# Kernel optimization log

Hardware: AMD Instinct MI355X
Metric: run time of the kernel (lower is better)

The kernel has to match this reference:

```python
import jax, jax.numpy as jnp
import numpy as np

B, S, H, L = 64, 512, 768, 9


def setup_inputs() -> dict:
    key = jax.random.key(0)
    ks = jax.random.split(key, 8)
    hidden = jax.random.normal(ks[0], (B, S, H), jnp.float32)
    lengths = jax.random.randint(ks[1], (B,), S // 2, S + 1)
    attention_mask = (jnp.arange(S)[None, :] < lengths[:, None]).astype(jnp.int32)
    labels = jax.random.randint(ks[2], (B, S), 0, L)
    # sprinkle some -100 ignore labels like HF datasets do
    ignore = jax.random.uniform(ks[3], (B, S)) < 0.05
    labels = jnp.where(ignore, -100, labels)
    W = jax.random.normal(ks[4], (H, L), jnp.float32) * 0.02
    b = jnp.zeros((L,), jnp.float32)
    start_transitions = jax.random.uniform(ks[5], (L,), jnp.float32, -0.1, 0.1)
    end_transitions = jax.random.uniform(ks[6], (L,), jnp.float32, -0.1, 0.1)
    transitions = jax.random.uniform(ks[7], (L, L), jnp.float32, -0.1, 0.1)
    return dict(hidden=hidden, attention_mask=attention_mask, labels=labels, W=W, b=b,
                start_transitions=start_transitions, end_transitions=end_transitions,
                transitions=transitions)


def _crf_numerator(emissions, tags, maskf, start_t, end_t, trans):
    # score of the gold tag sequence (torchcrf _compute_score)
    first = start_t[tags[:, 0]] + jnp.take_along_axis(emissions[:, 0], tags[:, 0:1], axis=1)[:, 0]
    em = jnp.take_along_axis(emissions, tags[..., None], axis=2)[..., 0]      # [B,S]
    tr = trans[tags[:, :-1], tags[:, 1:]]                                     # [B,S-1]
    score = first + jnp.sum((em[:, 1:] + tr) * maskf[:, 1:], axis=1)
    last_idx = (jnp.sum(maskf, axis=1).astype(jnp.int32) - 1)
    last_tags = jnp.take_along_axis(tags, last_idx[:, None], axis=1)[:, 0]
    return score + end_t[last_tags]


def _crf_lognorm(emissions, maskf, start_t, end_t, trans):
    # forward algorithm (torchcrf _compute_normalizer) as a lax.scan
    score0 = start_t[None, :] + emissions[:, 0]                               # [B,L]
    em_seq = jnp.transpose(emissions[:, 1:], (1, 0, 2))                       # [S-1,B,L]
    m_seq = maskf[:, 1:].T                                                    # [S-1,B]

    def step(score, xs):
        em_t, m_t = xs
        nxt = jax.nn.logsumexp(score[:, :, None] + trans[None] + em_t[:, None, :], axis=1)
        return jnp.where(m_t[:, None] > 0, nxt, score), None

    score, _ = jax.lax.scan(step, score0, (em_seq, m_seq))
    return jax.nn.logsumexp(score + end_t[None, :], axis=1)


def _viterbi(emissions, maskf, start_t, end_t, trans):
    score0 = start_t[None, :] + emissions[:, 0]                               # [B,L]
    em_seq = jnp.transpose(emissions[:, 1:], (1, 0, 2))
    m_seq = maskf[:, 1:].T

    def step(score, xs):
        em_t, m_t = xs
        cand = score[:, :, None] + trans[None]                                # [B,L,L]
        bp = jnp.argmax(cand, axis=1)                                         # [B,L]
        nxt = jnp.max(cand, axis=1) + em_t
        return jnp.where(m_t[:, None] > 0, nxt, score), bp

    score, history = jax.lax.scan(step, score0, (em_seq, m_seq))              # history [S-1,B,L]
    best_last = jnp.argmax(score + end_t[None, :], axis=1)                    # [B]

    def back(cur, xs):
        bp_t, m_t = xs
        prev = jnp.where(m_t > 0, jnp.take_along_axis(bp_t, cur[:, None], axis=1)[:, 0], cur)
        return prev, prev

    _, tags_rev = jax.lax.scan(back, best_last, (history[::-1], m_seq[::-1]))
    tags = jnp.concatenate([tags_rev[::-1].T, best_last[:, None]], axis=1)    # [B,S]
    return tags


def reference(hidden, attention_mask, labels, W, b, start_transitions, end_transitions, transitions):
    maskf = attention_mask.astype(hidden.dtype)                               # [B,S]
    logits = jnp.einsum('bsh,hl->bsl', hidden, W) + b                         # [B,S,L]
    safe_labels = jnp.where(labels == -100, 0, labels)
    num = _crf_numerator(logits, safe_labels, maskf, start_transitions, end_transitions, transitions)
    den = _crf_lognorm(logits, maskf, start_transitions, end_transitions, transitions)
    loss = -jnp.mean(num - den)                                               # -crf(..., reduction='mean')
    tags = _viterbi(logits, maskf, start_transitions, end_transitions, transitions)
    fake_logits = jax.nn.one_hot(tags, L, dtype=logits.dtype) * maskf[..., None]
    return loss, fake_logits
```

## Files before the change

### kernel.cpp

```cpp
#include <hip/hip_runtime.h>
#include <hip/hip_bf16.h>
#include <stdint.h>

constexpr int BB  = 64;
constexpr int SS  = 512;
constexpr int HH  = 768;
constexpr int NL  = 9;
constexpr int NROWS = BB * SS;
constexpr int EMN   = SS * NL;
constexpr float L2E = 1.4426950408889634f;
constexpr float LN2 = 0.6931471805599453f;

__device__ __forceinline__ float readlane_f(float v, int lane) {
  union { float f; int i; } u;
  u.f = v;
  u.i = __builtin_amdgcn_readlane(u.i, lane);
  return u.f;
}

__global__ __launch_bounds__(256, 2) void logits_kernel(
    const float* __restrict__ hidden, const float* __restrict__ W,
    const float* __restrict__ bias, float* __restrict__ logits) {
  const int lane = threadIdx.x & 63;
  const int wid  = blockIdx.x * 4 + (threadIdx.x >> 6);

  float w[3][4][NL];
#pragma unroll
  for (int j = 0; j < 3; ++j)
#pragma unroll
    for (int k = 0; k < 4; ++k) {
      const int r = lane * 4 + j * 256 + k;
#pragma unroll
      for (int l = 0; l < NL; ++l) w[j][k][l] = W[r * NL + l];
    }
  const float my_bias = (lane < NL) ? bias[lane] : 0.0f;

#pragma unroll
  for (int rep = 0; rep < 2; ++rep) {
    const int rA = wid + rep * 16384;
    const int rB = rA + 8192;
    const float4* hA = (const float4*)(hidden + (size_t)rA * HH);
    const float4* hB = (const float4*)(hidden + (size_t)rB * HH);
    float accA[NL], accB[NL];
#pragma unroll
    for (int l = 0; l < NL; ++l) { accA[l] = 0.0f; accB[l] = 0.0f; }
#pragma unroll
    for (int j = 0; j < 3; ++j) {
      const float4 a = hA[lane + j * 64];
      const float4 b = hB[lane + j * 64];
#pragma unroll
      for (int l = 0; l < NL; ++l) {
        accA[l] += a.x * w[j][0][l] + a.y * w[j][1][l] +
                   a.z * w[j][2][l] + a.w * w[j][3][l];
        accB[l] += b.x * w[j][0][l] + b.y * w[j][1][l] +
                   b.z * w[j][2][l] + b.w * w[j][3][l];
      }
    }
#pragma unroll
    for (int off = 32; off >= 1; off >>= 1)
#pragma unroll
      for (int l = 0; l < NL; ++l) {
        accA[l] += __shfl_xor(accA[l], off, 64);
        accB[l] += __shfl_xor(accB[l], off, 64);
      }
    if (lane < NL) {
      float vA = accA[0], vB = accB[0];
#pragma unroll
      for (int l = 1; l < NL; ++l)
        if (lane == l) { vA = accA[l]; vB = accB[l]; }
      logits[(size_t)rA * NL + lane] = vA + my_bias;
      logits[(size_t)rB * NL + lane] = vB + my_bias;
    }
  }
}

__global__ __launch_bounds__(64) void crf_kernel(
    const float* __restrict__ logits, const int* __restrict__ mask,
    const int* __restrict__ labels, const float* __restrict__ start_t,
    const float* __restrict__ end_t, const float* __restrict__ trans,
    float* __restrict__ out, float* __restrict__ num_den) {
  __shared__ __align__(16) float em_s[EMN + 16];
  __shared__ float tr_s[NL * NL];
  __shared__ int   lab[SS];
  __shared__ unsigned char bp_s[EMN + 80];
  __shared__ unsigned char tags_s[SS];
  __shared__ int   len_s;

  const int role = blockIdx.x >> 6;
  const int b    = blockIdx.x & 63;
  const int tid  = threadIdx.x;
  const float esc = (role == 0) ? L2E : 1.0f;

  {
    const float4* src = (const float4*)(logits + (size_t)b * EMN);
    float4* dst = (float4*)em_s;
    for (int i = tid; i < EMN / 4; i += 64) {
      float4 v = src[i];
      v.x *= esc; v.y *= esc; v.z *= esc; v.w *= esc;
      dst[i] = v;
    }
  }
  for (int i = tid; i < NL * NL; i += 64) tr_s[i] = trans[i] * esc;
  int lsum = 0;
  for (int t = tid; t < SS; t += 64) lsum += mask[b * SS + t];
#pragma unroll
  for (int off = 32; off >= 1; off >>= 1) lsum += __shfl_xor(lsum, off, 64);
  if (tid == 0) len_s = lsum;
  if (role == 2) {
    for (int t = tid; t < SS; t += 64) {
      const int v = labels[b * SS + t];
      lab[t] = (v == -100) ? 0 : v;
    }
  }
  __syncthreads();
  const int len = len_s;

  if (role == 0) {
    const int j = (tid < NL) ? tid : 0;
    float tcol[NL];
#pragma unroll
    for (int i = 0; i < NL; ++i) tcol[i] = tr_s[i * NL + j];
    float s[NL];
#pragma unroll
    for (int i = 0; i < NL; ++i) s[i] = start_t[i] * L2E + em_s[i];
    float emj = em_s[NL + j];
    for (int t = 1; t < len; ++t) {
      const float emj_n = em_s[(t + 1) * NL + j];
      float c[NL];
#pragma unroll
      for (int i = 0; i < NL; ++i) c[i] = s[i] + tcol[i];
      const float m01 = fmaxf(c[0], c[1]), m23 = fmaxf(c[2], c[3]);
      const float m45 = fmaxf(c[4], c[5]), m67 = fmaxf(c[6], c[7]);
      const float m = fmaxf(fmaxf(fmaxf(m01, m23), fmaxf(m45, m67)), c[8]);
      float p[NL];
#pragma unroll
      for (int i = 0; i < NL; ++i) p[i] = exp2f(c[i] - m);
      const float s01 = p[0] + p[1], s23 = p[2] + p[3];
      const float s45 = p[4] + p[5], s67 = p[6] + p[7];
      const float sum = ((s01 + s23) + (s45 + s67)) + p[8];
      const float nxt = m + __log2f(sum) + emj;
#pragma unroll
      for (int i = 0; i < NL; ++i) s[i] = readlane_f(nxt, i);
      emj = emj_n;
    }
    float c[NL];
#pragma unroll
    for (int i = 0; i < NL; ++i) c[i] = s[i] + end_t[i] * L2E;
    const float m01 = fmaxf(c[0], c[1]), m23 = fmaxf(c[2], c[3]);
    const float m45 = fmaxf(c[4], c[5]), m67 = fmaxf(c[6], c[7]);
    const float m = fmaxf(fmaxf(fmaxf(m01, m23), fmaxf(m45, m67)), c[8]);
    float sum = 0.0f;
#pragma unroll
    for (int i = 0; i < NL; ++i) sum += exp2f(c[i] - m);
    if (tid == 0) num_den[64 + b] = (m + __log2f(sum)) * LN2;

  } else if (role == 1) {
    const int j = (tid < NL) ? tid : 0;
    float tcol[NL];
#pragma unroll
    for (int i = 0; i < NL; ++i) tcol[i] = tr_s[i * NL + j];
    float s[NL];
#pragma unroll
    for (int i = 0; i < NL; ++i) s[i] = start_t[i] + em_s[i];
    float emj = em_s[NL + j];
    for (int t = 1; t < len; ++t) {
      const float emj_n = em_s[(t + 1) * NL + j];
      float c[NL];
#pragma unroll
      for (int i = 0; i < NL; ++i) c[i] = s[i] + tcol[i];
      const bool b01 = c[0] >= c[1], b23 = c[2] >= c[3];
      const bool b45 = c[4] >= c[5], b67 = c[6] >= c[7];
      const float v01 = b01 ? c[0] : c[1]; const int i01 = b01 ? 0 : 1;
      const float v23 = b23 ? c[2] : c[3]; const int i23 = b23 ? 2 : 3;
      const float v45 = b45 ? c[4] : c[5]; const int i45 = b45 ? 4 : 5;
      const float v67 = b67 ? c[6] : c[7]; const int i67 = b67 ? 6 : 7;
      const bool bA = v01 >= v23, bB = v45 >= v67;
      const float vA = bA ? v01 : v23; const int iA = bA ? i01 : i23;
      const float vB = bB ? v45 : v67; const int iB = bB ? i45 : i67;
      const bool bC = vA >= vB;
      const float vC = bC ? vA : vB; const int iC = bC ? iA : iB;
      const bool bD = vC >= c[8];
      const float best = bD ? vC : c[8];
      const int   arg  = bD ? iC : 8;
      bp_s[t * NL + tid] = (unsigned char)arg;
      const float nxt = best + emj;
#pragma unroll
      for (int i = 0; i < NL; ++i) s[i] = readlane_f(nxt, i);
      emj = emj_n;
    }
    float bv = s[0] + end_t[0];
    int   bl = 0;
#pragma unroll
    for (int i = 1; i < NL; ++i) {
      const float cc = s[i] + end_t[i];
      if (cc > bv) { bv = cc; bl = i; }
    }
    __syncthreads();

    uint64_t C = 0x876543210ULL;
#pragma unroll
    for (int k = 1; k <= 8; ++k) {
      const int t = 8 * tid + k;
      uint64_t nc = 0;
#pragma unroll
      for (int x = 0; x < 9; ++x) {
        const int g = bp_s[t * NL + x] & 15;
        nc |= ((C >> (4 * g)) & 15ULL) << (4 * x);
      }
      C = (t < len) ? nc : C;
    }
    const uint32_t Clo = (uint32_t)C, Chi = (uint32_t)(C >> 32);
    uint32_t cur = (uint32_t)bl;
    int bnd = 0;
#pragma unroll
    for (int c = 63; c >= 0; --c) {
      bnd = (tid == c) ? (int)cur : bnd;
      const uint32_t lo = (uint32_t)__builtin_amdgcn_readlane((int)Clo, c);
      const uint32_t hi = (uint32_t)__builtin_amdgcn_readlane((int)Chi, c);
      const uint64_t cc = ((uint64_t)hi << 32) | lo;
      cur = (uint32_t)((cc >> (4 * cur)) & 15u);
    }
    int tag = bnd;
#pragma unroll
    for (int k = 8; k >= 1; --k) {
      const int t = 8 * tid + k;
      const int tt = (t < 512) ? t : 511;
      const int nt = bp_s[tt * NL + tag];
      tag = (t < len) ? nt : tag;
      tags_s[t - 1] = (unsigned char)tag;
    }
    __syncthreads();
    for (int i = tid; i < EMN; i += 64) {
      const int t = i / NL;
      const int l = i - t * NL;
      out[1 + (size_t)b * EMN + i] =
          (t < len && l == (int)tags_s[t]) ? 1.0f : 0.0f;
    }

  } else {
    float contrib = 0.0f;
    for (int t = tid; t < SS; t += 64) {
      if (t >= 1 && t < len)
        contrib += em_s[t * NL + lab[t]] + tr_s[lab[t - 1] * NL + lab[t]];
    }
#pragma unroll
    for (int off = 32; off >= 1; off >>= 1)
      contrib += __shfl_xor(contrib, off, 64);
    if (tid == 0) {
      const int l0 = lab[0];
      num_den[b] = start_t[l0] + em_s[l0] + contrib + end_t[lab[len - 1]];
    }
  }
}

__global__ __launch_bounds__(64) void loss_kernel(
    const float* __restrict__ num_den, float* __restrict__ out) {
  const int tid = threadIdx.x;
  float v = num_den[64 + tid] - num_den[tid];
#pragma unroll
  for (int off = 32; off >= 1; off >>= 1) v += __shfl_xor(v, off, 64);
  if (tid == 0) out[0] = v * (1.0f / 64.0f);
}

extern "C" void kernel_launch(void* const* d_in, const int* in_sizes, int n_in,
                              void* d_out, int out_size, void* d_ws, size_t ws_size,
                              hipStream_t stream) {
  const float* hidden  = (const float*)d_in[0];
  const int*   mask    = (const int*)d_in[1];
  const int*   labels  = (const int*)d_in[2];
  const float* W       = (const float*)d_in[3];
  const float* bias    = (const float*)d_in[4];
  const float* start_t = (const float*)d_in[5];
  const float* end_t   = (const float*)d_in[6];
  const float* trans   = (const float*)d_in[7];
  float* out = (float*)d_out;

  float* logits  = (float*)d_ws;
  float* num_den = logits + (size_t)NROWS * NL;

  logits_kernel<<<2048, 256, 0, stream>>>(hidden, W, bias, logits);
  crf_kernel<<<192, 64, 0, stream>>>(logits, mask, labels, start_t, end_t,
                                     trans, out, num_den);
  loss_kernel<<<1, 64, 0, stream>>>(num_den, out);
}
```

Measured before the change: 292.0 us.

## Parallelize CRF forward algorithm via segmented log-semiring transfer matrices

The sequential forward (log-normalizer) scan is split into 8 segments per batch, each computed from 9 one-hot starting states in separate blocks. A new combine kernel chains the resulting 9x9 log-space transfer matrices, so the serial recurrence depth drops from about 512 steps to about 64. Sequence lengths are now computed inside the logits kernel. Emissions are read directly from global memory with a 4-deep register prefetch instead of being staged in LDS. The change adds roughly 4.6k extra blocks of redundant work and another kernel launch, and uses fast __expf/__logf instead of the exp2/log2 scaling.

```diff
diff --git a/kernel.cpp b/kernel.cpp
--- a/kernel.cpp
+++ b/kernel.cpp
@@ -8,8 +8,8 @@
 constexpr int NL  = 9;
 constexpr int NROWS = BB * SS;
 constexpr int EMN   = SS * NL;
-constexpr float L2E = 1.4426950408889634f;
-constexpr float LN2 = 0.6931471805599453f;
+constexpr int NSEG  = 8;
+constexpr float NEG  = -1e30f;
 
 __device__ __forceinline__ float readlane_f(float v, int lane) {
   union { float f; int i; } u;
@@ -20,9 +20,20 @@
 
 __global__ __launch_bounds__(256, 2) void logits_kernel(
     const float* __restrict__ hidden, const float* __restrict__ W,
-    const float* __restrict__ bias, float* __restrict__ logits) {
+    const float* __restrict__ bias, const int* __restrict__ mask,
+    float* __restrict__ logits, int* __restrict__ lens) {
   const int lane = threadIdx.x & 63;
   const int wid  = blockIdx.x * 4 + (threadIdx.x >> 6);
+
+  if (blockIdx.x < 64 && threadIdx.x < 64) {
+    const int4* mp = (const int4*)(mask + blockIdx.x * SS);
+    const int4 a = mp[threadIdx.x];
+    const int4 c = mp[threadIdx.x + 64];
+    int lsum = a.x + a.y + a.z + a.w + c.x + c.y + c.z + c.w;
+#pragma unroll
+    for (int off = 32; off >= 1; off >>= 1) lsum += __shfl_xor(lsum, off, 64);
+    if (threadIdx.x == 0) lens[blockIdx.x] = lsum;
+  }
 
   float w[3][4][NL];
 #pragma unroll
@@ -74,119 +85,60 @@
   }
 }
 
-__global__ __launch_bounds__(64) void crf_kernel(
-    const float* __restrict__ logits, const int* __restrict__ mask,
-    const int* __restrict__ labels, const float* __restrict__ start_t,
-    const float* __restrict__ end_t, const float* __restrict__ trans,
-    float* __restrict__ out, float* __restrict__ num_den) {
-  __shared__ __align__(16) float em_s[EMN + 16];
-  __shared__ float tr_s[NL * NL];
-  __shared__ int   lab[SS];
+__global__ __launch_bounds__(64) void scan_kernel(
+    const float* __restrict__ logits, const int* __restrict__ labels,
+    const float* __restrict__ start_t, const float* __restrict__ end_t,
+    const float* __restrict__ trans, float* __restrict__ out,
+    float* __restrict__ num_den, const int* __restrict__ lens,
+    float* __restrict__ segmat) {
   __shared__ unsigned char bp_s[EMN + 80];
   __shared__ unsigned char tags_s[SS];
-  __shared__ int   len_s;
-
-  const int role = blockIdx.x >> 6;
-  const int b    = blockIdx.x & 63;
-  const int tid  = threadIdx.x;
-  const float esc = (role == 0) ? L2E : 1.0f;
-
-  {
-    const float4* src = (const float4*)(logits + (size_t)b * EMN);
-    float4* dst = (float4*)em_s;
-    for (int i = tid; i < EMN / 4; i += 64) {
-      float4 v = src[i];
-      v.x *= esc; v.y *= esc; v.z *= esc; v.w *= esc;
-      dst[i] = v;
-    }
-  }
-  for (int i = tid; i < NL * NL; i += 64) tr_s[i] = trans[i] * esc;
-  int lsum = 0;
-  for (int t = tid; t < SS; t += 64) lsum += mask[b * SS + t];
-#pragma unroll
-  for (int off = 32; off >= 1; off >>= 1) lsum += __shfl_xor(lsum, off, 64);
-  if (tid == 0) len_s = lsum;
-  if (role == 2) {
-    for (int t = tid; t < SS; t += 64) {
-      const int v = labels[b * SS + t];
-      lab[t] = (v == -100) ? 0 : v;
-    }
-  }
-  __syncthreads();
-  const int len = len_s;
-
-  if (role == 0) {
-    const int j = (tid < NL) ? tid : 0;
-    float tcol[NL];
-#pragma unroll
-    for (int i = 0; i < NL; ++i) tcol[i] = tr_s[i * NL + j];
+  __shared__ int lab[SS];
+
+  const int blk = blockIdx.x;
+  const int tid = threadIdx.x;
+  const int j   = (tid < NL) ? tid : NL - 1;
+
+  if (blk < 64) {
+    const int b   = blk;
+    const int len = lens[b];
+    const float* emb = logits + (size_t)b * EMN;
+    float tc[NL];
+#pragma unroll
+    for (int i = 0; i < NL; ++i) tc[i] = trans[i * NL + j];
     float s[NL];
 #pragma unroll
-    for (int i = 0; i < NL; ++i) s[i] = start_t[i] * L2E + em_s[i];
-    float emj = em_s[NL + j];
+    for (int i = 0; i < NL; ++i) s[i] = start_t[i] + emb[i];
+    float eA = emb[1 * NL + j], eB = emb[2 * NL + j];
+    float eC = emb[3 * NL + j], eD = emb[4 * NL + j];
     for (int t = 1; t < len; ++t) {
-      const float emj_n = em_s[(t + 1) * NL + j];
       float c[NL];
 #pragma unroll
-      for (int i = 0; i < NL; ++i) c[i] = s[i] + tcol[i];
-      const float m01 = fmaxf(c[0], c[1]), m23 = fmaxf(c[2], c[3]);
-      const float m45 = fmaxf(c[4], c[5]), m67 = fmaxf(c[6], c[7]);
-      const float m = fmaxf(fmaxf(fmaxf(m01, m23), fmaxf(m45, m67)), c[8]);
-      float p[NL];
-#pragma unroll
-      for (int i = 0; i < NL; ++i) p[i] = exp2f(c[i] - m);
-      const float s01 = p[0] + p[1], s23 = p[2] + p[3];
-      const float s45 = p[4] + p[5], s67 = p[6] + p[7];
-      const float sum = ((s01 + s23) + (s45 + s67)) + p[8];
-      const float nxt = m + __log2f(sum) + emj;
+      for (int i = 0; i < NL; ++i) c[i] = s[i] + tc[i];
+      const float x01 = fmaxf(c[0], c[1]), x23 = fmaxf(c[2], c[3]);
+      const float x45 = fmaxf(c[4], c[5]), x67 = fmaxf(c[6], c[7]);
+      const float best = fmaxf(fmaxf(fmaxf(x01, x23), fmaxf(x45, x67)), c[8]);
+      const float nxt = best + eA;
+      {
+        const bool b01 = c[0] >= c[1], b23 = c[2] >= c[3];
+        const bool b45 = c[4] >= c[5], b67 = c[6] >= c[7];
+        const float v01 = b01 ? c[0] : c[1]; const int i01 = b01 ? 0 : 1;
+        const float v23 = b23 ? c[2] : c[3]; const int i23 = b23 ? 2 : 3;
+        const float v45 = b45 ? c[4] : c[5]; const int i45 = b45 ? 4 : 5;
+        const float v67 = b67 ? c[6] : c[7]; const int i67 = b67 ? 6 : 7;
+        const bool bA = v01 >= v23, bB = v45 >= v67;
+        const float vA = bA ? v01 : v23; const int iA = bA ? i01 : i23;
+        const float vB = bB ? v45 : v67; const int iB = bB ? i45 : i67;
+        const bool bC = vA >= vB;
+        const float vC = bC ? vA : vB; const int iC = bC ? iA : iB;
+        const bool bD = vC >= c[8];
+        const int arg = bD ? iC : 8;
+        bp_s[t * NL + tid] = (unsigned char)arg;
+      }
 #pragma unroll
       for (int i = 0; i < NL; ++i) s[i] = readlane_f(nxt, i);
-      emj = emj_n;
-    }
-    float c[NL];
-#pragma unroll
-    for (int i = 0; i < NL; ++i) c[i] = s[i] + end_t[i] * L2E;
-    const float m01 = fmaxf(c[0], c[1]), m23 = fmaxf(c[2], c[3]);
-    const float m45 = fmaxf(c[4], c[5]), m67 = fmaxf(c[6], c[7]);
-    const float m = fmaxf(fmaxf(fmaxf(m01, m23), fmaxf(m45, m67)), c[8]);
-    float sum = 0.0f;
-#pragma unroll
-    for (int i = 0; i < NL; ++i) sum += exp2f(c[i] - m);
-    if (tid == 0) num_den[64 + b] = (m + __log2f(sum)) * LN2;
-
-  } else if (role == 1) {
-    const int j = (tid < NL) ? tid : 0;
-    float tcol[NL];
-#pragma unroll
-    for (int i = 0; i < NL; ++i) tcol[i] = tr_s[i * NL + j];
-    float s[NL];
-#pragma unroll
-    for (int i = 0; i < NL; ++i) s[i] = start_t[i] + em_s[i];
-    float emj = em_s[NL + j];
-    for (int t = 1; t < len; ++t) {
-      const float emj_n = em_s[(t + 1) * NL + j];
-      float c[NL];
-#pragma unroll
-      for (int i = 0; i < NL; ++i) c[i] = s[i] + tcol[i];
-      const bool b01 = c[0] >= c[1], b23 = c[2] >= c[3];
-      const bool b45 = c[4] >= c[5], b67 = c[6] >= c[7];
-      const float v01 = b01 ? c[0] : c[1]; const int i01 = b01 ? 0 : 1;
-      const float v23 = b23 ? c[2] : c[3]; const int i23 = b23 ? 2 : 3;
-      const float v45 = b45 ? c[4] : c[5]; const int i45 = b45 ? 4 : 5;
-      const float v67 = b67 ? c[6] : c[7]; const int i67 = b67 ? 6 : 7;
-      const bool bA = v01 >= v23, bB = v45 >= v67;
-      const float vA = bA ? v01 : v23; const int iA = bA ? i01 : i23;
-      const float vB = bB ? v45 : v67; const int iB = bB ? i45 : i67;
-      const bool bC = vA >= vB;
-      const float vC = bC ? vA : vB; const int iC = bC ? iA : iB;
-      const bool bD = vC >= c[8];
-      const float best = bD ? vC : c[8];
-      const int   arg  = bD ? iC : 8;
-      bp_s[t * NL + tid] = (unsigned char)arg;
-      const float nxt = best + emj;
-#pragma unroll
-      for (int i = 0; i < NL; ++i) s[i] = readlane_f(nxt, i);
-      emj = emj_n;
+      eA = eB; eB = eC; eC = eD;
+      eD = emb[(t + 4) * NL + j];
     }
     float bv = s[0] + end_t[0];
     int   bl = 0;
@@ -237,20 +189,117 @@
           (t < len && l == (int)tags_s[t]) ? 1.0f : 0.0f;
     }
 
-  } else {
+  } else if (blk < 128) {
+    const int b   = blk - 64;
+    const int len = lens[b];
+    const float* emb = logits + (size_t)b * EMN;
+    for (int t = tid; t < SS; t += 64) {
+      const int v = labels[b * SS + t];
+      lab[t] = (v == -100) ? 0 : v;
+    }
+    __syncthreads();
     float contrib = 0.0f;
     for (int t = tid; t < SS; t += 64) {
       if (t >= 1 && t < len)
-        contrib += em_s[t * NL + lab[t]] + tr_s[lab[t - 1] * NL + lab[t]];
+        contrib += emb[t * NL + lab[t]] + trans[lab[t - 1] * NL + lab[t]];
     }
 #pragma unroll
     for (int off = 32; off >= 1; off >>= 1)
       contrib += __shfl_xor(contrib, off, 64);
     if (tid == 0) {
       const int l0 = lab[0];
-      num_den[b] = start_t[l0] + em_s[l0] + contrib + end_t[lab[len - 1]];
-    }
-  }
+      num_den[b] = start_t[l0] + emb[l0] + contrib + end_t[lab[len - 1]];
+    }
+
+  } else {
+    const int id  = blk - 128;
+    const int b   = id / 72;
+    const int rem = id - b * 72;
+    const int sg  = rem / 9;
+    const int e   = rem - sg * 9;
+    const int len = lens[b];
+    const float* emb = logits + (size_t)b * EMN;
+    float tc[NL];
+#pragma unroll
+    for (int i = 0; i < NL; ++i) tc[i] = trans[i * NL + j];
+    float s[NL];
+#pragma unroll
+    for (int i = 0; i < NL; ++i) s[i] = (i == e) ? 0.0f : NEG;
+    float my = (j == e) ? 0.0f : NEG;
+    const int tbeg = 64 * sg + 1;
+    const int tlast = (64 * sg + 64 < 511) ? 64 * sg + 64 : 511;
+    float eA = emb[tbeg * NL + j],       eB = emb[(tbeg + 1) * NL + j];
+    float eC = emb[(tbeg + 2) * NL + j], eD = emb[(tbeg + 3) * NL + j];
+    for (int t = tbeg; t <= tlast; ++t) {
+      if (t >= len) break;
+      float c[NL];
+#pragma unroll
+      for (int i = 0; i < NL; ++i) c[i] = s[i] + tc[i];
+      const float x01 = fmaxf(c[0], c[1]), x23 = fmaxf(c[2], c[3]);
+      const float x45 = fmaxf(c[4], c[5]), x67 = fmaxf(c[6], c[7]);
+      const float m = fmaxf(fmaxf(fmaxf(x01, x23), fmaxf(x45, x67)), c[8]);
+      float sum = 0.0f;
+#pragma unroll
+      for (int i = 0; i < NL; ++i) sum += __expf(c[i] - m);
+      const float nxt = m + __logf(sum) + eA;
+      my = nxt;
+#pragma unroll
+      for (int i = 0; i < NL; ++i) s[i] = readlane_f(nxt, i);
+      eA = eB; eB = eC; eC = eD;
+      eD = emb[(t + 4) * NL + j];
+    }
+    if (tid < NL)
+      segmat[((size_t)(b * NSEG + sg) * NL + e) * NL + tid] = my;
+  }
+}
+
+__global__ __launch_bounds__(64) void combine_kernel(
+    const float* __restrict__ logits, const float* __restrict__ segmat,
+    const float* __restrict__ start_t, const float* __restrict__ end_t,
+    float* __restrict__ num_den) {
+  const int b   = blockIdx.x;
+  const int tid = threadIdx.x;
+  const int j   = (tid < NL) ? tid : NL - 1;
+  float s[NL];
+#pragma unroll
+  for (int i = 0; i < NL; ++i) s[i] = start_t[i] + logits[(size_t)b * EMN + i];
+  float mcur[NL], mnxt[NL];
+  {
+    const float* M = segmat + (size_t)(b * NSEG) * 81;
+#pragma unroll
+    for (int i = 0; i < NL; ++i) mcur[i] = M[i * NL + j];
+  }
+  for (int sg = 0; sg < NSEG; ++sg) {
+    if (sg + 1 < NSEG) {
+      const float* M = segmat + (size_t)(b * NSEG + sg + 1) * 81;
+#pragma unroll
+      for (int i = 0; i < NL; ++i) mnxt[i] = M[i * NL + j];
+    }
+    float c[NL];
+#pragma unroll
+    for (int i = 0; i < NL; ++i) c[i] = s[i] + mcur[i];
+    const float x01 = fmaxf(c[0], c[1]), x23 = fmaxf(c[2], c[3]);
+    const float x45 = fmaxf(c[4], c[5]), x67 = fmaxf(c[6], c[7]);
+    const float m = fmaxf(fmaxf(fmaxf(x01, x23), fmaxf(x45, x67)), c[8]);
+    float sum = 0.0f;
+#pragma unroll
+    for (int i = 0; i < NL; ++i) sum += __expf(c[i] - m);
+    const float nxt = m + __logf(sum);
+#pragma unroll
+    for (int i = 0; i < NL; ++i) s[i] = readlane_f(nxt, i);
+#pragma unroll
+    for (int i = 0; i < NL; ++i) mcur[i] = mnxt[i];
+  }
+  float c[NL];
+#pragma unroll
+  for (int i = 0; i < NL; ++i) c[i] = s[i] + end_t[i];
+  const float x01 = fmaxf(c[0], c[1]), x23 = fmaxf(c[2], c[3]);
+  const float x45 = fmaxf(c[4], c[5]), x67 = fmaxf(c[6], c[7]);
+  const float m = fmaxf(fmaxf(fmaxf(x01, x23), fmaxf(x45, x67)), c[8]);
+  float sum = 0.0f;
+#pragma unroll
+  for (int i = 0; i < NL; ++i) sum += __expf(c[i] - m);
+  if (tid == 0) num_den[64 + b] = m + __logf(sum);
 }
 
 __global__ __launch_bounds__(64) void loss_kernel(
@@ -276,10 +325,13 @@
   float* out = (float*)d_out;
 
   float* logits  = (float*)d_ws;
-  float* num_den = logits + (size_t)NROWS * NL;
-
-  logits_kernel<<<2048, 256, 0, stream>>>(hidden, W, bias, logits);
-  crf_kernel<<<192, 64, 0, stream>>>(logits, mask, labels, start_t, end_t,
-                                     trans, out, num_den);
+  float* segmat  = logits + (size_t)NROWS * NL;
+  float* num_den = segmat + (size_t)BB * NSEG * 81;
+  int*   lens    = (int*)(num_den + 128);
+
+  logits_kernel<<<2048, 256, 0, stream>>>(hidden, W, bias, mask, logits, lens);
+  scan_kernel<<<4736, 64, 0, stream>>>(logits, labels, start_t, end_t, trans,
+                                       out, num_den, lens, segmat);
+  combine_kernel<<<64, 64, 0, stream>>>(logits, segmat, start_t, end_t, num_den);
   loss_kernel<<<1, 64, 0, stream>>>(num_den, out);
 }
```

Result: faster. 259.5 us (-11.1%).
